# Kernel tuning notes

Measured on AMD Instinct MI355X. Metric: run time of the kernel, lower is better.

The kernel has to match this reference:

```python
import jax, jax.numpy as jnp
import numpy as np

CODEC_RANGE = 1.0
COMMIT_WEIGHT = 0.1


def setup_inputs() -> dict:
    key = jax.random.key(0)
    ks = jax.random.split(key, 6)
    B, T, D, Dc, NQ, BINS = 8, 4096, 512, 256, 8, 1024
    return {
        "x": jax.random.normal(ks[0], (B, T, D), dtype=jnp.float32),
        "in_w": jax.random.normal(ks[1], (Dc, D), dtype=jnp.float32) * (1.0 / np.sqrt(D)),
        "in_b": jnp.zeros((Dc,), dtype=jnp.float32),
        "out_w": jax.random.normal(ks[2], (D, Dc), dtype=jnp.float32) * (1.0 / np.sqrt(Dc)),
        "out_b": jnp.zeros((D,), dtype=jnp.float32),
        "codebooks": jax.random.normal(ks[3], (NQ, BINS, Dc), dtype=jnp.float32),
    }


def reference(x, in_w, in_b, out_w, out_b, codebooks):
    # input projection + tanh range limiting
    h = jnp.tanh(x @ in_w.T + in_b) * CODEC_RANGE  # [B, T, Dc]

    def step(residual, codebook):
        # squared L2 distances: ||r||^2 - 2 r.e + ||e||^2  -> [B, T, bins]
        r2 = jnp.sum(residual * residual, axis=-1, keepdims=True)
        e2 = jnp.sum(codebook * codebook, axis=-1)  # [bins]
        dist = r2 - 2.0 * jnp.einsum("btd,nd->btn", residual, codebook) + e2
        idx = jnp.argmin(dist, axis=-1)  # [B, T]
        q = codebook[idx]  # gather -> [B, T, Dc]
        # commitment loss vs. detached quantized vectors
        commit = jnp.mean((jax.lax.stop_gradient(q) - residual) ** 2)
        return residual - q, (q, idx, commit)

    _, (qs, idxs, commits) = jax.lax.scan(step, h, codebooks)
    quantized = jnp.sum(qs, axis=0)  # [B, T, Dc]
    # straight-through estimator
    quantized = h + jax.lax.stop_gradient(quantized - h)
    out = quantized @ out_w.T + out_b  # [B, T, D]
    commit_loss = COMMIT_WEIGHT * jnp.sum(commits)
    return out, idxs, commit_loss
```

## Files before the change

### kernel.cpp

```cpp
#include <hip/hip_runtime.h>
#include <math.h>

#define DC 256
#define NBINS 1024
#define NQ 8
#define NTOK 32768
#define D_IN 512
#define DCH 32
#define TOK 64
#define STG_BLOCKS (NTOK / TOK)
#define MARGIN 5e-3f

typedef __attribute__((ext_vector_type(8))) short short8v;
typedef __attribute__((ext_vector_type(4))) float f32x4;

__device__ __forceinline__ unsigned short f2bf(float x) {
  unsigned u = __float_as_uint(x);
  return (unsigned short)((u + 0x7fffu + ((u >> 16) & 1u)) >> 16);
}
__device__ __forceinline__ float bf2f(unsigned short h) {
  return __uint_as_float(((unsigned)h) << 16);
}
__device__ __forceinline__ void store8s(unsigned short* dst, const unsigned short* v) {
  uint4 u;
  u.x = v[0] | ((unsigned)v[1] << 16); u.y = v[2] | ((unsigned)v[3] << 16);
  u.z = v[4] | ((unsigned)v[5] << 16); u.w = v[6] | ((unsigned)v[7] << 16);
  *reinterpret_cast<uint4*>(dst) = u;
}
__device__ __forceinline__ short8v load8s(const unsigned short* p) {
  return __builtin_bit_cast(short8v, *reinterpret_cast<const float4*>(p));
}

__device__ __forceinline__ float np_sumsq128(const float* a) {
#pragma clang fp contract(off)
  float r0 = a[0] * a[0], r1 = a[1] * a[1], r2 = a[2] * a[2], r3 = a[3] * a[3];
  float r4 = a[4] * a[4], r5 = a[5] * a[5], r6 = a[6] * a[6], r7 = a[7] * a[7];
  for (int i = 8; i < 128; i += 8) {
    r0 += a[i + 0] * a[i + 0]; r1 += a[i + 1] * a[i + 1];
    r2 += a[i + 2] * a[i + 2]; r3 += a[i + 3] * a[i + 3];
    r4 += a[i + 4] * a[i + 4]; r5 += a[i + 5] * a[i + 5];
    r6 += a[i + 6] * a[i + 6]; r7 += a[i + 7] * a[i + 7];
  }
  return ((r0 + r1) + (r2 + r3)) + ((r4 + r5) + (r6 + r7));
}
__device__ __forceinline__ float np_sumsq256(const float* a) {
#pragma clang fp contract(off)
  float lo = np_sumsq128(a);
  float hi = np_sumsq128(a + 128);
  return lo + hi;
}

__global__ void e2_np_kernel(const float* __restrict__ cb, float* __restrict__ e2) {
  int b = blockIdx.x * 256 + threadIdx.x;
  e2[b] = np_sumsq256(cb + (size_t)b * DC);
}

__global__ void presplit_kernel(const float* __restrict__ cb,
                                unsigned short* __restrict__ cb_h,
                                unsigned short* __restrict__ cb_l) {
  int id = blockIdx.x * 256 + threadIdx.x;
  int sk = id >> 10, bin = id & 1023;
  int s = sk >> 5, k8 = sk & 31;
  const float* src = cb + ((size_t)s * NBINS + bin) * DC + k8 * 8;
  unsigned short hh[8], ll[8];
#pragma unroll
  for (int j = 0; j < 8; ++j) {
    float x = src[j];
    unsigned short h = f2bf(x);
    hh[j] = h;
    ll[j] = f2bf(x - bf2f(h));
  }
  store8s(cb_h + (size_t)id * 8, hh);
  store8s(cb_l + (size_t)id * 8, ll);
}

__global__ __launch_bounds__(256) void in_proj_kernel(
    const float* __restrict__ x, const float* __restrict__ in_w,
    const float* __restrict__ in_b, float* __restrict__ res) {
  __shared__ __align__(16) float aT[DCH][68];
  __shared__ __align__(16) float bT[DCH][68];
  const int thr = threadIdx.x;
  const int tx = thr & 15, ty = thr >> 4;
  const int m0 = blockIdx.x * 64, n0 = blockIdx.y * 64;
  float acc[4][4] = {};
  float s1[4][4] = {};
  for (int kc = 0; kc < D_IN; kc += DCH) {
    if (kc == 384) {
#pragma unroll
      for (int i = 0; i < 4; ++i)
#pragma unroll
        for (int j = 0; j < 4; ++j) { s1[i][j] = acc[i][j]; acc[i][j] = 0.f; }
    }
    __syncthreads();
#pragma unroll
    for (int i = 0; i < 2; ++i) {
      int q = thr + 256 * i;
      int m = q >> 3, kk = (q & 7) << 2;
      float4 v = *reinterpret_cast<const float4*>(x + (size_t)(m0 + m) * D_IN + kc + kk);
      aT[kk + 0][m] = v.x; aT[kk + 1][m] = v.y; aT[kk + 2][m] = v.z; aT[kk + 3][m] = v.w;
      float4 w = *reinterpret_cast<const float4*>(in_w + (size_t)(n0 + m) * D_IN + kc + kk);
      bT[kk + 0][m] = w.x; bT[kk + 1][m] = w.y; bT[kk + 2][m] = w.z; bT[kk + 3][m] = w.w;
    }
    __syncthreads();
#pragma unroll 8
    for (int d = 0; d < DCH; ++d) {
      float4 a = *reinterpret_cast<const float4*>(&aT[d][ty * 4]);
      float4 b = *reinterpret_cast<const float4*>(&bT[d][tx * 4]);
      float av[4] = {a.x, a.y, a.z, a.w};
      float bv[4] = {b.x, b.y, b.z, b.w};
#pragma unroll
      for (int i = 0; i < 4; ++i)
#pragma unroll
        for (int j = 0; j < 4; ++j) acc[i][j] = fmaf(av[i], bv[j], acc[i][j]);
    }
  }
#pragma unroll
  for (int i = 0; i < 4; ++i) {
    int m = m0 + ty * 4 + i, n = n0 + tx * 4;
    float4 hv;
#pragma unroll
    for (int j = 0; j < 4; ++j) {
#pragma clang fp contract(off)
      float c = s1[i][j] + acc[i][j];
      float pre = c + in_b[n + j];
      ((float*)&hv)[j] = tanhf(pre);
    }
    *reinterpret_cast<float4*>(res + (size_t)m * DC + n) = hv;
  }
}

__global__ __launch_bounds__(256, 2) void stage_kernel(
    const float* __restrict__ cb, const float* __restrict__ e2,
    const unsigned short* __restrict__ cb_h, const unsigned short* __restrict__ cb_l,
    float* __restrict__ res, float* __restrict__ idx_f, double* __restrict__ partial,
    int s) {
  __shared__ __align__(16) unsigned short a_hi[32 * 64 * 8];
  __shared__ __align__(16) unsigned short a_lo[32 * 64 * 8];
  __shared__ float m1s[4 * 64], m2s[4 * 64];
  __shared__ int   i1s[4 * 64];
  __shared__ int   win_l[64], flag_l[64];
  __shared__ __align__(16) float rrow_s[256];
  __shared__ float redf[4];
  __shared__ int   redi[4];
  __shared__ double wsum[4];

  const int thr = threadIdx.x;
  const int lane = thr & 63;
  const int w = thr >> 6;
  const int lg = lane >> 4;
  const int lc = lane & 15;
  const int m0 = blockIdx.x * TOK;
  const float* cbs = cb + (size_t)s * NBINS * DC;
  const float* e2s = e2 + (size_t)s * NBINS;
  const unsigned short* bhp = cb_h + (size_t)s * (32 * 1024 * 8);
  const unsigned short* blp = cb_l + (size_t)s * (32 * 1024 * 8);
  double sqacc = 0.0;

  {
    int row = thr >> 2, d0 = (thr & 3) << 6;
    const float* rrow = res + (size_t)(m0 + row) * DC + d0;
#pragma unroll
    for (int c = 0; c < 8; ++c) {
      float4 r0 = *reinterpret_cast<const float4*>(rrow + c * 8);
      float4 r1 = *reinterpret_cast<const float4*>(rrow + c * 8 + 4);
      float rv[8] = {r0.x, r0.y, r0.z, r0.w, r1.x, r1.y, r1.z, r1.w};
      unsigned short hh[8], ll[8];
#pragma unroll
      for (int j = 0; j < 8; ++j) {
        float xv = -2.0f * rv[j];
        unsigned short h = f2bf(xv);
        hh[j] = h; ll[j] = f2bf(xv - bf2f(h));
      }
      int k8 = (d0 >> 3) + c;
      store8s(a_hi + ((size_t)k8 * 64 + row) * 8, hh);
      store8s(a_lo + ((size_t)k8 * 64 + row) * 8, ll);
    }
  }
  m1s[thr] = 3.4028235e38f; m2s[thr] = 3.4028235e38f; i1s[thr] = 0;
  __syncthreads();

  for (int c = 0; c < 4; ++c) {
    const int bbase = w * 256 + c * 64;
    f32x4 acc[4][4];
#pragma unroll
    for (int nt = 0; nt < 4; ++nt) {
      float ev = e2s[bbase + nt * 16 + lc];
      f32x4 iv = {ev, ev, ev, ev};
#pragma unroll
      for (int rt = 0; rt < 4; ++rt) acc[rt][nt] = iv;
    }
#pragma unroll 2
    for (int kstep = 0; kstep < 8; ++kstep) {
      short8v ah[4], al[4];
#pragma unroll
      for (int rt = 0; rt < 4; ++rt) {
        int off = ((kstep * 4 + lg) * 64 + rt * 16 + lc) * 8;
        ah[rt] = load8s(a_hi + off);
        al[rt] = load8s(a_lo + off);
      }
      short8v bh[4], bl[4];
#pragma unroll
      for (int nt = 0; nt < 4; ++nt) {
        size_t boff = ((size_t)(kstep * 4 + lg) * 1024 + bbase + nt * 16 + lc) * 8;
        bh[nt] = load8s(bhp + boff);
        bl[nt] = load8s(blp + boff);
      }
#pragma unroll
      for (int nt = 0; nt < 4; ++nt)
#pragma unroll
        for (int rt = 0; rt < 4; ++rt)
          acc[rt][nt] = __builtin_amdgcn_mfma_f32_16x16x32_bf16(ah[rt], bh[nt], acc[rt][nt], 0, 0, 0);
#pragma unroll
      for (int nt = 0; nt < 4; ++nt)
#pragma unroll
        for (int rt = 0; rt < 4; ++rt)
          acc[rt][nt] = __builtin_amdgcn_mfma_f32_16x16x32_bf16(ah[rt], bl[nt], acc[rt][nt], 0, 0, 0);
#pragma unroll
      for (int nt = 0; nt < 4; ++nt)
#pragma unroll
        for (int rt = 0; rt < 4; ++rt)
          acc[rt][nt] = __builtin_amdgcn_mfma_f32_16x16x32_bf16(al[rt], bh[nt], acc[rt][nt], 0, 0, 0);
    }
#pragma unroll
    for (int rt = 0; rt < 4; ++rt)
#pragma unroll
      for (int reg = 0; reg < 4; ++reg) {
        float m1 = 3.4028235e38f, m2 = 3.4028235e38f; int i1 = 0;
#pragma unroll
        for (int nt = 0; nt < 4; ++nt) {
          float v = acc[rt][nt][reg];
          int b = bbase + nt * 16 + lc;
          if (v < m1) { m2 = m1; m1 = v; i1 = b; }
          else m2 = fminf(m2, v);
        }
#pragma unroll
        for (int msk = 1; msk < 16; msk <<= 1) {
          float om1 = __shfl_xor(m1, msk, 64);
          float om2 = __shfl_xor(m2, msk, 64);
          int   oi1 = __shfl_xor(i1, msk, 64);
          if (om1 < m1 || (om1 == m1 && oi1 < i1)) { m2 = fminf(m1, om2); m1 = om1; i1 = oi1; }
          else m2 = fminf(m2, om1);
        }
        if (lc == 0) {
          int sidx = w * 64 + rt * 16 + lg * 4 + reg;
          float pm1 = m1s[sidx], pm2 = m2s[sidx]; int pi1 = i1s[sidx];
          if (m1 < pm1 || (m1 == pm1 && i1 < pi1)) {
            m1s[sidx] = m1; m2s[sidx] = fminf(pm1, m2); i1s[sidx] = i1;
          } else {
            m2s[sidx] = fminf(pm2, m1);
          }
        }
      }
  }
  __syncthreads();
  if (thr < TOK) {
    float m1 = m1s[thr], m2 = m2s[thr]; int i1 = i1s[thr];
#pragma unroll
    for (int ww = 1; ww < 4; ++ww) {
      float om1 = m1s[ww * 64 + thr], om2 = m2s[ww * 64 + thr];
      int oi1 = i1s[ww * 64 + thr];
      if (om1 < m1 || (om1 == m1 && oi1 < i1)) { m2 = fminf(m1, om2); m1 = om1; i1 = oi1; }
      else m2 = fminf(m2, om1);
    }
    win_l[thr] = i1;
    flag_l[thr] = (m2 - m1 < MARGIN) ? 1 : 0;
  }
  __syncthreads();
  for (int row = 0; row < TOK; ++row) {
    if (!flag_l[row]) continue;
    if (thr < 64)
      reinterpret_cast<float4*>(rrow_s)[thr] =
          reinterpret_cast<const float4*>(res + (size_t)(m0 + row) * DC)[thr];
    __syncthreads();
    float r2 = np_sumsq256(rrow_s);
    float best = 3.4028235e38f; int bb = 0;
#pragma unroll
    for (int jj = 0; jj < 4; ++jj) {
      int b = thr * 4 + jj;
      const float4* e4 = reinterpret_cast<const float4*>(cbs + (size_t)b * DC);
      const float4* r4 = reinterpret_cast<const float4*>(rrow_s);
      float accv = 0.f;
      for (int q = 0; q < 64; ++q) {
        float4 ev = e4[q], rv = r4[q];
        accv = fmaf(rv.x, ev.x, accv);
        accv = fmaf(rv.y, ev.y, accv);
        accv = fmaf(rv.z, ev.z, accv);
        accv = fmaf(rv.w, ev.w, accv);
      }
      {
#pragma clang fp contract(off)
        float t = r2 - 2.0f * accv;
        float dist = t + e2s[b];
        if (dist < best) { best = dist; bb = b; }
      }
    }
#pragma unroll
    for (int msk = 1; msk < 64; msk <<= 1) {
      float ov = __shfl_xor(best, msk, 64);
      int   ob = __shfl_xor(bb, msk, 64);
      if (ov < best || (ov == best && ob < bb)) { best = ov; bb = ob; }
    }
    if (lane == 0) { redf[w] = best; redi[w] = bb; }
    __syncthreads();
    if (thr == 0) {
      float bs = redf[0]; int bfin = redi[0];
#pragma unroll
      for (int ww = 1; ww < 4; ++ww)
        if (redf[ww] < bs || (redf[ww] == bs && redi[ww] < bfin)) { bs = redf[ww]; bfin = redi[ww]; }
      win_l[row] = bfin;
    }
    __syncthreads();
  }
  {
    int row = thr >> 2, d0 = (thr & 3) << 6;
    int wbin = win_l[row];
    const float* erow = cbs + (size_t)wbin * DC + d0;
    float* rrow = res + (size_t)(m0 + row) * DC + d0;
#pragma unroll
    for (int c = 0; c < 8; ++c) {
      float4 r0 = *reinterpret_cast<const float4*>(rrow + c * 8);
      float4 r1 = *reinterpret_cast<const float4*>(rrow + c * 8 + 4);
      float4 e0 = *reinterpret_cast<const float4*>(erow + c * 8);
      float4 e1 = *reinterpret_cast<const float4*>(erow + c * 8 + 4);
      float nv[8] = {r0.x - e0.x, r0.y - e0.y, r0.z - e0.z, r0.w - e0.w,
                     r1.x - e1.x, r1.y - e1.y, r1.z - e1.z, r1.w - e1.w};
#pragma unroll
      for (int j = 0; j < 8; ++j) sqacc += (double)nv[j] * nv[j];
      *reinterpret_cast<float4*>(rrow + c * 8) = (float4){nv[0], nv[1], nv[2], nv[3]};
      *reinterpret_cast<float4*>(rrow + c * 8 + 4) = (float4){nv[4], nv[5], nv[6], nv[7]};
    }
    if (thr < TOK) idx_f[(size_t)s * NTOK + m0 + thr] = (float)win_l[thr];
  }
#pragma unroll
  for (int msk = 1; msk < 64; msk <<= 1) sqacc += __shfl_xor(sqacc, msk, 64);
  if (lane == 0) wsum[w] = sqacc;
  __syncthreads();
  if (thr == 0) {
    double t = 0.0;
#pragma unroll
    for (int ww = 0; ww < 4; ++ww) t += wsum[ww];
    partial[(size_t)s * STG_BLOCKS + blockIdx.x] = t;
  }
}

__global__ void finalize_kernel(const double* __restrict__ partial, float* __restrict__ out_last) {
  __shared__ double acc_s[64];
  int t = threadIdx.x;
  double a = 0.0;
  for (int i = 0; i < 64; ++i) a += partial[(size_t)t * 64 + i];
  acc_s[t] = a;
  __syncthreads();
  if (t == 0) {
    double tot = 0.0;
    for (int i = 0; i < 64; ++i) tot += acc_s[i];
    out_last[0] = (float)(0.1 * tot / 8388608.0);
  }
}

__global__ __launch_bounds__(256) void out_proj_kernel(
    const float* __restrict__ cb, const float* __restrict__ idx_f,
    const float* __restrict__ out_w, const float* __restrict__ out_b,
    float* __restrict__ out) {
  __shared__ __align__(16) float aT[DCH][68];
  __shared__ __align__(16) float bT[DCH][68];
  __shared__ int idx_l[NQ][64];
  const int thr = threadIdx.x;
  const int tx = thr & 15, ty = thr >> 4;
  const int m0 = blockIdx.x * 64, n0 = blockIdx.y * 64;
#pragma unroll
  for (int i = 0; i < 2; ++i) {
    int q = thr + 256 * i;
    int s = q >> 6, m = q & 63;
    idx_l[s][m] = (int)idx_f[(size_t)s * NTOK + m0 + m];
  }
  float acc[4][4] = {};
  for (int kc = 0; kc < DC; kc += DCH) {
    __syncthreads();
#pragma unroll
    for (int i = 0; i < 2; ++i) {
      int q = thr + 256 * i;
      int m = q >> 3, kk = (q & 7) << 2;
      float4 v = {0.f, 0.f, 0.f, 0.f};
#pragma unroll
      for (int s = 0; s < NQ; ++s) {
        const float4 e = *reinterpret_cast<const float4*>(
            cb + ((size_t)s * NBINS + idx_l[s][m]) * DC + kc + kk);
        v.x += e.x; v.y += e.y; v.z += e.z; v.w += e.w;
      }
      aT[kk + 0][m] = v.x; aT[kk + 1][m] = v.y; aT[kk + 2][m] = v.z; aT[kk + 3][m] = v.w;
      float4 wv = *reinterpret_cast<const float4*>(out_w + (size_t)(n0 + m) * DC + kc + kk);
      bT[kk + 0][m] = wv.x; bT[kk + 1][m] = wv.y; bT[kk + 2][m] = wv.z; bT[kk + 3][m] = wv.w;
    }
    __syncthreads();
#pragma unroll 8
    for (int d = 0; d < DCH; ++d) {
      float4 a = *reinterpret_cast<const float4*>(&aT[d][ty * 4]);
      float4 b = *reinterpret_cast<const float4*>(&bT[d][tx * 4]);
      float av[4] = {a.x, a.y, a.z, a.w};
      float bv[4] = {b.x, b.y, b.z, b.w};
#pragma unroll
      for (int i = 0; i < 4; ++i)
#pragma unroll
        for (int j = 0; j < 4; ++j) acc[i][j] = fmaf(av[i], bv[j], acc[i][j]);
    }
  }
#pragma unroll
  for (int i = 0; i < 4; ++i) {
    int m = m0 + ty * 4 + i, n = n0 + tx * 4;
    float4 o;
    o.x = acc[i][0] + out_b[n + 0];
    o.y = acc[i][1] + out_b[n + 1];
    o.z = acc[i][2] + out_b[n + 2];
    o.w = acc[i][3] + out_b[n + 3];
    *reinterpret_cast<float4*>(out + (size_t)m * D_IN + n) = o;
  }
}

extern "C" void kernel_launch(void* const* d_in, const int* in_sizes, int n_in,
                              void* d_out, int out_size, void* d_ws, size_t ws_size,
                              hipStream_t stream) {
  (void)in_sizes; (void)n_in; (void)out_size; (void)d_ws; (void)ws_size;
  const float* x     = (const float*)d_in[0];
  const float* in_w  = (const float*)d_in[1];
  const float* in_b  = (const float*)d_in[2];
  const float* out_w = (const float*)d_in[3];
  const float* out_b = (const float*)d_in[4];
  const float* cb    = (const float*)d_in[5];
  float* out = (float*)d_out;
  float* res    = out;
  float* e2     = out + 8388608;
  double* part  = (double*)(out + 8404992);
  unsigned short* cb_h = (unsigned short*)(out + 9000000);
  unsigned short* cb_l = (unsigned short*)(out + 10500000);
  float* idx_f  = out + 16777216;
  float* c_out  = out + 17039360;

  hipLaunchKernelGGL(e2_np_kernel, dim3(32), dim3(256), 0, stream, cb, e2);
  hipLaunchKernelGGL(presplit_kernel, dim3(1024), dim3(256), 0, stream, cb, cb_h, cb_l);
  hipLaunchKernelGGL(in_proj_kernel, dim3(512, 4), dim3(256), 0, stream, x, in_w, in_b, res);
  for (int s = 0; s < NQ; ++s) {
    hipLaunchKernelGGL(stage_kernel, dim3(STG_BLOCKS), dim3(256), 0, stream,
                       cb, e2, cb_h, cb_l, res, idx_f, part, s);
  }
  hipLaunchKernelGGL(finalize_kernel, dim3(1), dim3(64), 0, stream, part, c_out);
  hipLaunchKernelGGL(out_proj_kernel, dim3(512, 8), dim3(256), 0, stream, cb, idx_f, out_w, out_b, out);
}
```

Before: 1.691 ms.

## Split stage kernel into MFMA scoring kernel and exact-fix/update kernel

Splits the per-stage kernel into a score kernel (bf16-split MFMA distances, top-2 tracking) that writes winner and ambiguity flags to global memory, and a separate fix kernel that does exact fp32 rescoring of flagged rows, residual update and loss accumulation. The intent is to shrink register and LDS pressure in each kernel so the MFMA part and the fix-up part can each get better occupancy. In exchange it doubles the launches per stage and adds a global round trip for winners and flags.

```diff
diff --git a/kernel.cpp b/kernel.cpp
--- a/kernel.cpp
+++ b/kernel.cpp
@@ -129,20 +129,15 @@
   }
 }
 
-__global__ __launch_bounds__(256, 2) void stage_kernel(
-    const float* __restrict__ cb, const float* __restrict__ e2,
+__global__ __launch_bounds__(256, 2) void score_kernel(
+    const float* __restrict__ e2,
     const unsigned short* __restrict__ cb_h, const unsigned short* __restrict__ cb_l,
-    float* __restrict__ res, float* __restrict__ idx_f, double* __restrict__ partial,
+    const float* __restrict__ res, int* __restrict__ win_g, int* __restrict__ flag_g,
     int s) {
-  __shared__ __align__(16) unsigned short a_hi[32 * 64 * 8];
-  __shared__ __align__(16) unsigned short a_lo[32 * 64 * 8];
-  __shared__ float m1s[4 * 64], m2s[4 * 64];
-  __shared__ int   i1s[4 * 64];
-  __shared__ int   win_l[64], flag_l[64];
-  __shared__ __align__(16) float rrow_s[256];
-  __shared__ float redf[4];
-  __shared__ int   redi[4];
-  __shared__ double wsum[4];
+  __shared__ __align__(16) unsigned short a_hi[32 * TOK * 8];
+  __shared__ __align__(16) unsigned short a_lo[32 * TOK * 8];
+  __shared__ float m1s[4 * TOK], m2s[4 * TOK];
+  __shared__ int   i1s[4 * TOK];
 
   const int thr = threadIdx.x;
   const int lane = thr & 63;
@@ -150,11 +145,9 @@
   const int lg = lane >> 4;
   const int lc = lane & 15;
   const int m0 = blockIdx.x * TOK;
-  const float* cbs = cb + (size_t)s * NBINS * DC;
   const float* e2s = e2 + (size_t)s * NBINS;
   const unsigned short* bhp = cb_h + (size_t)s * (32 * 1024 * 8);
   const unsigned short* blp = cb_l + (size_t)s * (32 * 1024 * 8);
-  double sqacc = 0.0;
 
   {
     int row = thr >> 2, d0 = (thr & 3) << 6;
@@ -172,8 +165,8 @@
         hh[j] = h; ll[j] = f2bf(xv - bf2f(h));
       }
       int k8 = (d0 >> 3) + c;
-      store8s(a_hi + ((size_t)k8 * 64 + row) * 8, hh);
-      store8s(a_lo + ((size_t)k8 * 64 + row) * 8, ll);
+      store8s(a_hi + ((size_t)k8 * TOK + row) * 8, hh);
+      store8s(a_lo + ((size_t)k8 * TOK + row) * 8, ll);
     }
   }
   m1s[thr] = 3.4028235e38f; m2s[thr] = 3.4028235e38f; i1s[thr] = 0;
@@ -194,7 +187,7 @@
       short8v ah[4], al[4];
 #pragma unroll
       for (int rt = 0; rt < 4; ++rt) {
-        int off = ((kstep * 4 + lg) * 64 + rt * 16 + lc) * 8;
+        int off = ((kstep * 4 + lg) * TOK + rt * 16 + lc) * 8;
         ah[rt] = load8s(a_hi + off);
         al[rt] = load8s(a_lo + off);
       }
@@ -242,7 +235,7 @@
           else m2 = fminf(m2, om1);
         }
         if (lc == 0) {
-          int sidx = w * 64 + rt * 16 + lg * 4 + reg;
+          int sidx = w * TOK + rt * 16 + lg * 4 + reg;
           float pm1 = m1s[sidx], pm2 = m2s[sidx]; int pi1 = i1s[sidx];
           if (m1 < pm1 || (m1 == pm1 && i1 < pi1)) {
             m1s[sidx] = m1; m2s[sidx] = fminf(pm1, m2); i1s[sidx] = i1;
@@ -257,14 +250,35 @@
     float m1 = m1s[thr], m2 = m2s[thr]; int i1 = i1s[thr];
 #pragma unroll
     for (int ww = 1; ww < 4; ++ww) {
-      float om1 = m1s[ww * 64 + thr], om2 = m2s[ww * 64 + thr];
-      int oi1 = i1s[ww * 64 + thr];
+      float om1 = m1s[ww * TOK + thr], om2 = m2s[ww * TOK + thr];
+      int oi1 = i1s[ww * TOK + thr];
       if (om1 < m1 || (om1 == m1 && oi1 < i1)) { m2 = fminf(m1, om2); m1 = om1; i1 = oi1; }
       else m2 = fminf(m2, om1);
     }
-    win_l[thr] = i1;
-    flag_l[thr] = (m2 - m1 < MARGIN) ? 1 : 0;
-  }
+    win_g[m0 + thr] = i1;
+    flag_g[m0 + thr] = (m2 - m1 < MARGIN) ? 1 : 0;
+  }
+}
+
+__global__ __launch_bounds__(256) void fix_kernel(
+    const float* __restrict__ cb, const float* __restrict__ e2,
+    const int* __restrict__ win_g, const int* __restrict__ flag_g,
+    float* __restrict__ res, float* __restrict__ idx_f, double* __restrict__ partial,
+    int s) {
+  __shared__ int win_l[TOK], flag_l[TOK];
+  __shared__ __align__(16) float rrow_s[256];
+  __shared__ float redf[4];
+  __shared__ int   redi[4];
+  __shared__ double wsum[4];
+  const int thr = threadIdx.x;
+  const int lane = thr & 63;
+  const int w = thr >> 6;
+  const int m0 = blockIdx.x * TOK;
+  const float* cbs = cb + (size_t)s * NBINS * DC;
+  const float* e2s = e2 + (size_t)s * NBINS;
+  double sqacc = 0.0;
+
+  if (thr < TOK) { win_l[thr] = win_g[m0 + thr]; flag_l[thr] = flag_g[m0 + thr]; }
   __syncthreads();
   for (int row = 0; row < TOK; ++row) {
     if (!flag_l[row]) continue;
@@ -432,6 +446,8 @@
   double* part  = (double*)(out + 8404992);
   unsigned short* cb_h = (unsigned short*)(out + 9000000);
   unsigned short* cb_l = (unsigned short*)(out + 10500000);
+  int* win_g   = (int*)(out + 11600000);
+  int* flag_g  = (int*)(out + 11700000);
   float* idx_f  = out + 16777216;
   float* c_out  = out + 17039360;
 
@@ -439,8 +455,10 @@
   hipLaunchKernelGGL(presplit_kernel, dim3(1024), dim3(256), 0, stream, cb, cb_h, cb_l);
   hipLaunchKernelGGL(in_proj_kernel, dim3(512, 4), dim3(256), 0, stream, x, in_w, in_b, res);
   for (int s = 0; s < NQ; ++s) {
-    hipLaunchKernelGGL(stage_kernel, dim3(STG_BLOCKS), dim3(256), 0, stream,
-                       cb, e2, cb_h, cb_l, res, idx_f, part, s);
+    hipLaunchKernelGGL(score_kernel, dim3(STG_BLOCKS), dim3(256), 0, stream,
+                       e2, cb_h, cb_l, res, win_g, flag_g, s);
+    hipLaunchKernelGGL(fix_kernel, dim3(STG_BLOCKS), dim3(256), 0, stream,
+                       cb, e2, win_g, flag_g, res, idx_f, part, s);
   }
   hipLaunchKernelGGL(finalize_kernel, dim3(1), dim3(64), 0, stream, part, c_out);
   hipLaunchKernelGGL(out_proj_kernel, dim3(512, 8), dim3(256), 0, stream, cb, idx_f, out_w, out_b, out);
```

Measured after the change: 1.562 ms. -7.7%, faster.
